# Kernel optimization log

Hardware: AMD Instinct MI355X
Metric: run time of the kernel (lower is better)

## Reference

```python
import jax, jax.numpy as jnp
import numpy as np

B, INP, OUP, FGROUP, H, W = 32, 256, 256, 8, 64, 64
CG = INP // FGROUP  # channels per group in GLGF fc1 layers


def conv3x3(x, w):
    # x: (N,1,H,W), w: (1,1,3,3); stride 1, padding 1 (SAME)
    return jax.lax.conv_general_dilated(
        x, w, window_strides=(1, 1), padding='SAME',
        dimension_numbers=('NCHW', 'OIHW', 'NCHW'))


def setup_inputs() -> dict:
    key = jax.random.key(0)
    ks = jax.random.split(key, 8)
    return {
        'x': jax.random.normal(ks[0], (B, INP, H, W), dtype=jnp.float32),
        # GLGF params (all 1x1 convs, bias=False), stored as dense matrices
        'w1l': jax.random.normal(ks[1], (FGROUP, CG, CG), dtype=jnp.float32) * 0.05,   # wn_fc1_l (groups=fgroup)
        'w1g1': jax.random.normal(ks[2], (FGROUP, CG), dtype=jnp.float32) * 0.05,      # wn_fc1_g1 (inp->fgroup, groups=fgroup)
        'w1g2': jax.random.normal(ks[3], (INP, FGROUP), dtype=jnp.float32) * 0.05,     # wn_fc1_g2 (fgroup->inp dense)
        'w2l': jax.random.normal(ks[4], (INP, OUP), dtype=jnp.float32) * 0.05,         # wn_fc2_l (groups=inp): input ch i -> oup outputs
        'w2g': jax.random.normal(ks[5], (INP,), dtype=jnp.float32) * 0.05,             # wn_fc2_g (inp->1 dense)
        'conv1_w': jax.random.normal(ks[6], (1, 1, 3, 3), dtype=jnp.float32) * 0.1,
        'conv2_w': jax.random.normal(ks[7], (1, 1, 3, 3), dtype=jnp.float32) * 0.1,
    }


def reference(x, w1l, w1g1, w1g2, w2l, w2g, conv1_w, conv2_w):
    b, c, h, w_ = x.shape
    fgroup, cg, _ = w1l.shape
    oup = w2l.shape[1]

    # adaptive_avg_pool2d(x, (1,1)) -> (B, inp) descriptor
    g = x.mean(axis=(2, 3))                                   # (B, inp)
    gg = g.reshape(b, fgroup, cg)

    # GLGF: fc1_l (grouped) + fc1_g2(fc1_g1) (squeeze to fgroup then expand)
    local = jnp.einsum('bgi,goi->bgo', gg, w1l).reshape(b, c)  # (B, inp)
    glob = jnp.einsum('bgi,gi->bg', gg, w1g1) @ w1g2.T         # (B, inp)
    s = jax.nn.sigmoid(local + glob)                           # (B, inp)

    # fc2_l (groups=inp): torch channel order is (input_ch g, out j) -> g*oup + j
    # fc2_g adds a per-sample scalar to every channel
    xw = s[:, :, None] * w2l + (s @ w2g)[:, None, None]        # (B, inp, oup)
    # WA_1Conv reinterprets the flat (oup*inp) channels as (oup, inp)
    Wdyn = xw.reshape(b, oup, c)                               # (B, oup, inp)

    # grouped conv with groups=batch, ksize=1 == per-sample matmul
    y = jnp.einsum('bihw,boi->bohw', x, Wdyn)                  # (B, oup, H, W)

    # channel gating: mean over channels -> conv3x3 -> sigmoid -> conv3x3
    cmap = y.mean(axis=1, keepdims=True)                       # (B, 1, H, W)
    cmap = conv3x3(cmap, conv1_w)
    cmap = jax.nn.sigmoid(cmap)
    cmap = conv3x3(cmap, conv2_w)
    return y * cmap
```

## Files before the change

### kernel.cpp

```cpp
#include <hip/hip_runtime.h>
#include <hip/hip_bf16.h>

typedef float  f32x4  __attribute__((ext_vector_type(4)));
typedef short  bf16x8 __attribute__((ext_vector_type(8)));

__device__ __forceinline__ short f2bf(float f) {
    union { __hip_bfloat16 h; short s; } u;
    u.h = __float2bfloat16(f);
    return u.s;
}

__device__ __forceinline__ void gload_lds16(const void* g, void* l) {
    __builtin_amdgcn_global_load_lds(
        (const __attribute__((address_space(1))) unsigned int*)g,
        (__attribute__((address_space(3))) unsigned int*)l, 16, 0, 0);
}

__device__ __forceinline__ void nt_load8(const float* p, float* dst) {
    const f32x4* vp = reinterpret_cast<const f32x4*>(p);
    f32x4 a = __builtin_nontemporal_load(vp);
    f32x4 b = __builtin_nontemporal_load(vp + 1);
    *reinterpret_cast<f32x4*>(dst)     = a;
    *reinterpret_cast<f32x4*>(dst + 4) = b;
}

__global__ __launch_bounds__(256) void transpose_kernel(const float* __restrict__ x,
                                                        short* __restrict__ xt,
                                                        float* __restrict__ gpart,
                                                        float* __restrict__ xsump) {
    const int pchunk = blockIdx.x;
    const int cchunk = blockIdx.y;
    const int c0 = cchunk * 64;
    const int b  = blockIdx.z;
    const int tid = threadIdx.x;
    const int cpair = tid >> 3;
    const int poct  = tid & 7;
    const int p0 = pchunk * 64;

    __shared__ unsigned int tile[64 * 32];
    __shared__ float xred[4 * 64];

    const float* rowA = x + ((size_t)(b * 256 + c0 + 2 * cpair)) * 4096 + p0 + poct * 8;
    const float* rowB = rowA + 4096;
    float av[8], bv[8];
    nt_load8(rowA, av);
    nt_load8(rowB, bv);

    float sA = 0.f, sB = 0.f;
    #pragma unroll
    for (int e = 0; e < 8; ++e) { sA += av[e]; sB += bv[e]; }
    sA += __shfl_xor(sA, 1, 64); sA += __shfl_xor(sA, 2, 64); sA += __shfl_xor(sA, 4, 64);
    sB += __shfl_xor(sB, 1, 64); sB += __shfl_xor(sB, 2, 64); sB += __shfl_xor(sB, 4, 64);
    if (poct == 0) {
        gpart[((size_t)(b * 256 + c0 + 2 * cpair)) * 64 + pchunk] = sA;
        gpart[((size_t)(b * 256 + c0 + 2 * cpair + 1)) * 64 + pchunk] = sB;
    }

    float xs[8];
    #pragma unroll
    for (int e = 0; e < 8; ++e) {
        float v = av[e] + bv[e];
        v += __shfl_xor(v, 8, 64);
        v += __shfl_xor(v, 16, 64);
        v += __shfl_xor(v, 32, 64);
        xs[e] = v;
    }
    if ((tid & 56) == 0) {
        int wv = tid >> 6;
        #pragma unroll
        for (int e = 0; e < 8; ++e) xred[wv * 64 + poct * 8 + e] = xs[e];
    }

    const int s = cpair >> 2, w = cpair & 3;
    #pragma unroll
    for (int e = 0; e < 8; ++e) {
        int p = poct * 8 + e;
        unsigned int u = (unsigned int)(unsigned short)f2bf(av[e]) |
                         ((unsigned int)(unsigned short)f2bf(bv[e]) << 16);
        tile[p * 32 + ((s ^ poct) << 2) + w] = u;
    }
    __syncthreads();

    if (tid < 64) {
        float v = xred[tid] + xred[64 + tid] + xred[128 + tid] + xred[192 + tid];
        xsump[((size_t)(cchunk * 32 + b)) * 4096 + p0 + tid] = v;
    }

    const int so = tid & 7;
    #pragma unroll
    for (int h = 0; h < 2; ++h) {
        int p = (tid >> 3) + h * 32;
        int sp = so ^ ((p >> 3) & 7);
        uint4 v = *reinterpret_cast<const uint4*>(&tile[p * 32 + sp * 4]);
        *reinterpret_cast<uint4*>(xt + ((size_t)b * 4096 + p0 + p) * 256 + c0 + so * 8) = v;
    }
}

__global__ __launch_bounds__(256) void prep_kernel(
    const float* __restrict__ gpart, const float* __restrict__ w1l,
    const float* __restrict__ w1g1, const float* __restrict__ w1g2,
    const float* __restrict__ w2l, const float* __restrict__ w2g,
    float* __restrict__ s_out, float* __restrict__ t_out,
    float* __restrict__ vq_out, short* __restrict__ w2l_bf) {
    int b = blockIdx.x;
    int tid = threadIdx.x;
    if (b >= 32) {
        int seg = b - 32;
        const float* src = w2l + seg * 4096;
        short* dst = w2l_bf + seg * 4096;
        #pragma unroll
        for (int it = 0; it < 4; ++it) {
            float4 v = *reinterpret_cast<const float4*>(src + it * 1024 + tid * 4);
            short4 o;
            o.x = f2bf(v.x); o.y = f2bf(v.y); o.z = f2bf(v.z); o.w = f2bf(v.w);
            *reinterpret_cast<short4*>(dst + it * 1024 + tid * 4) = o;
        }
        return;
    }
    __shared__ float gs[256];
    __shared__ float zs[8];
    __shared__ float ss[256];
    __shared__ float red[4];
    {
        const float4* gp = reinterpret_cast<const float4*>(gpart + (size_t)(b * 256 + tid) * 64);
        float acc = 0.f;
        #pragma unroll
        for (int j = 0; j < 16; ++j) { float4 v = gp[j]; acc += v.x + v.y + v.z + v.w; }
        gs[tid] = acc * (1.0f / 4096.0f);
    }
    __syncthreads();
    if (tid < 8) {
        float z = 0.f;
        for (int i = 0; i < 32; ++i) z += gs[tid * 32 + i] * w1g1[tid * 32 + i];
        zs[tid] = z;
    }
    __syncthreads();
    int grp = tid >> 5, o = tid & 31;
    float local = 0.f;
    #pragma unroll 4
    for (int i = 0; i < 32; ++i) local += gs[grp * 32 + i] * w1l[grp * 1024 + o * 32 + i];
    float glob = 0.f;
    #pragma unroll
    for (int gg = 0; gg < 8; ++gg) glob += zs[gg] * w1g2[tid * 8 + gg];
    float sv = 1.0f / (1.0f + expf(-(local + glob)));
    ss[tid] = sv;
    s_out[b * 256 + tid] = sv;
    float tv = sv * w2g[tid];
    #pragma unroll
    for (int off = 32; off; off >>= 1) tv += __shfl_down(tv, off, 64);
    if ((tid & 63) == 0) red[tid >> 6] = tv;
    __syncthreads();
    float tb = red[0] + red[1] + red[2] + red[3];
    if (tid == 0) t_out[b] = tb;
    float v = 0.f;
    for (int o2 = 0; o2 < 256; ++o2) v += ss[o2] * w2l[o2 * 256 + tid];
    vq_out[b * 256 + tid] = v * (1.0f / 256.0f);
}

__global__ __launch_bounds__(256) void cmap0_kernel(const short* __restrict__ xt,
                                                    const float* __restrict__ vq,
                                                    const float* __restrict__ t,
                                                    const float* __restrict__ xsump,
                                                    float* __restrict__ cmap0,
                                                    float* __restrict__ txs) {
    const int b = blockIdx.y;
    const int p = blockIdx.x * 256 + threadIdx.x;
    __shared__ float vs[256];
    vs[threadIdx.x] = vq[b * 256 + threadIdx.x];
    __syncthreads();
    const uint4* row = reinterpret_cast<const uint4*>(xt + ((size_t)b * 4096 + p) * 256);
    float acc = 0.f;
    #pragma unroll 8
    for (int it = 0; it < 32; ++it) {
        uint4 u = row[it];
        const unsigned int* uw = reinterpret_cast<const unsigned int*>(&u);
        #pragma unroll
        for (int j = 0; j < 4; ++j) {
            unsigned int wrd = uw[j];
            union { unsigned int u; float f; } lo, hi;
            lo.u = wrd << 16;
            hi.u = wrd & 0xffff0000u;
            acc += lo.f * vs[it * 8 + 2 * j] + hi.f * vs[it * 8 + 2 * j + 1];
        }
    }
    float xs = 0.f;
    #pragma unroll
    for (int part = 0; part < 4; ++part)
        xs += xsump[((size_t)(part * 32 + b)) * 4096 + p];
    float tb = t[b];
    float tx = tb * xs;
    cmap0[b * 4096 + p] = acc + tx;
    txs[b * 4096 + p] = tx;
}

__global__ __launch_bounds__(256) void convs_kernel(const float* __restrict__ cmap0,
                                                    const float* __restrict__ w9a,
                                                    const float* __restrict__ w9b,
                                                    float* __restrict__ cmap) {
    const int strip = blockIdx.x;
    const int b = blockIdx.y;
    const int tid = threadIdx.x;
    const int r0 = strip * 8;
    const int rlo = (r0 == 0) ? 0 : r0 - 1;
    const int rhi = (r0 + 8 > 63) ? 63 : r0 + 8;
    const int cnt = rhi - rlo + 1;

    __shared__ float mid[10 * 64];
    float wa[9], wb[9];
    #pragma unroll
    for (int i = 0; i < 9; ++i) { wa[i] = w9a[i]; wb[i] = w9b[i]; }
    const float* ib = cmap0 + (size_t)b * 4096;

    for (int idx = tid; idx < cnt * 64; idx += 256) {
        int r = rlo + (idx >> 6), cc = idx & 63;
        float acc = 0.f;
        #pragma unroll
        for (int dy = -1; dy <= 1; ++dy)
            #pragma unroll
            for (int dx = -1; dx <= 1; ++dx) {
                int rr = r + dy, xx = cc + dx;
                if (rr >= 0 && rr < 64 && xx >= 0 && xx < 64)
                    acc += ib[rr * 64 + xx] * wa[(dy + 1) * 3 + (dx + 1)];
            }
        mid[idx] = 1.0f / (1.0f + expf(-acc));
    }
    __syncthreads();
    for (int idx = tid; idx < 512; idx += 256) {
        int r = r0 + (idx >> 6), cc = idx & 63;
        float acc = 0.f;
        #pragma unroll
        for (int dy = -1; dy <= 1; ++dy)
            #pragma unroll
            for (int dx = -1; dx <= 1; ++dx) {
                int rr = r + dy, xx = cc + dx;
                if (rr >= 0 && rr < 64 && xx >= 0 && xx < 64)
                    acc += mid[(rr - rlo) * 64 + xx] * wb[(dy + 1) * 3 + (dx + 1)];
            }
        cmap[(size_t)b * 4096 + r * 64 + cc] = acc;
    }
}

__global__ __launch_bounds__(512) void gemm_epi_kernel(
    const short* __restrict__ xt, const short* __restrict__ w2l_bf,
    const float* __restrict__ s, const float* __restrict__ txs,
    const float* __restrict__ cmap, float* __restrict__ out) {
    const int b  = blockIdx.z;
    const int p0 = blockIdx.x * 64;
    const int tid  = threadIdx.x;
    const int lane = tid & 63;
    const int w    = tid >> 6;
    const int wm = w >> 1, wn = w & 1;

    __shared__ short Alds[2][256 * 64];
    __shared__ short Xlds[2][64 * 64];

    const int sl   = (lane & 7) ^ (lane >> 3);
    const int lrow = lane >> 3;

    float txr[2], cmr[2], sv[4][4];
    #pragma unroll
    for (int n = 0; n < 2; ++n) {
        int p = p0 + wn * 32 + n * 16 + (lane & 15);
        txr[n] = txs[b * 4096 + p];
        cmr[n] = cmap[b * 4096 + p];
    }
    #pragma unroll
    for (int m = 0; m < 4; ++m)
        #pragma unroll
        for (int r = 0; r < 4; ++r)
            sv[m][r] = s[b * 256 + wm * 64 + m * 16 + (lane >> 4) * 4 + r];

    f32x4 acc[4][2] = {};

    auto STAGE = [&](int bi, int ks) {
        #pragma unroll
        for (int j = 0; j < 4; ++j) {
            int chunk = w * 4 + j;
            int row = chunk * 8 + lrow;
            gload_lds16(w2l_bf + (size_t)row * 256 + ks + sl * 8,
                        (char*)(&Alds[bi][0]) + chunk * 1024);
        }
        int prow = w * 8 + lrow;
        gload_lds16(xt + ((size_t)b * 4096 + p0 + prow) * 256 + ks + sl * 8,
                    (char*)(&Xlds[bi][0]) + w * 1024);
    };

    STAGE(0, 0);
    #pragma unroll
    for (int t = 0; t < 4; ++t) {
        const int bi = t & 1;
        if (t < 3) {
            STAGE(bi ^ 1, (t + 1) * 64);
            asm volatile("s_waitcnt vmcnt(5)" ::: "memory");
        } else {
            asm volatile("s_waitcnt vmcnt(0)" ::: "memory");
        }
        __builtin_amdgcn_s_barrier();
        asm volatile("" ::: "memory");
        #pragma unroll
        for (int kk = 0; kk < 2; ++kk) {
            bf16x8 af[4], bfr[2];
            const int ss = kk * 4 + (lane >> 4);
            #pragma unroll
            for (int m = 0; m < 4; ++m) {
                int o = wm * 64 + m * 16 + (lane & 15);
                af[m] = *reinterpret_cast<const bf16x8*>(
                    (char*)(&Alds[bi][0]) + o * 128 + ((ss ^ (lane & 7)) * 16));
            }
            #pragma unroll
            for (int n = 0; n < 2; ++n) {
                int p = wn * 32 + n * 16 + (lane & 15);
                bfr[n] = *reinterpret_cast<const bf16x8*>(
                    (char*)(&Xlds[bi][0]) + p * 128 + ((ss ^ (lane & 7)) * 16));
            }
            #pragma unroll
            for (int m = 0; m < 4; ++m)
                #pragma unroll
                for (int n = 0; n < 2; ++n)
                    acc[m][n] = __builtin_amdgcn_mfma_f32_16x16x32_bf16(af[m], bfr[n], acc[m][n], 0, 0, 0);
        }
        asm volatile("" ::: "memory");
        __builtin_amdgcn_s_barrier();
    }
    #pragma unroll
    for (int n = 0; n < 2; ++n) {
        int p = p0 + wn * 32 + n * 16 + (lane & 15);
        #pragma unroll
        for (int m = 0; m < 4; ++m) {
            #pragma unroll
            for (int r = 0; r < 4; ++r) {
                int o = wm * 64 + m * 16 + (lane >> 4) * 4 + r;
                float yv = (sv[m][r] * acc[m][n][r] + txr[n]) * cmr[n];
                __builtin_nontemporal_store(yv, &out[((size_t)b * 256 + o) * 4096 + p]);
            }
        }
    }
}

extern "C" void kernel_launch(void* const* d_in, const int* in_sizes, int n_in,
                              void* d_out, int out_size, void* d_ws, size_t ws_size,
                              hipStream_t stream) {
    const float* x       = (const float*)d_in[0];
    const float* w1l     = (const float*)d_in[1];
    const float* w1g1    = (const float*)d_in[2];
    const float* w1g2    = (const float*)d_in[3];
    const float* w2l     = (const float*)d_in[4];
    const float* w2g     = (const float*)d_in[5];
    const float* conv1_w = (const float*)d_in[6];
    const float* conv2_w = (const float*)d_in[7];
    float* out = (float*)d_out;

    float* wsf    = (float*)d_ws;
    float* s      = wsf;
    float* t      = wsf + 8192;
    float* vq     = wsf + 8256;
    float* cmap0  = wsf + 16448;
    float* txs    = wsf + 147520;
    float* cmap   = wsf + 278592;
    float* gpart  = wsf + 409664;
    float* xsump  = wsf + 933952;
    short* w2l_bf = (short*)(wsf + 1458240);
    short* xt     = (short*)(wsf + 1491008);

    transpose_kernel<<<dim3(64, 4, 32), 256, 0, stream>>>(x, xt, gpart, xsump);
    prep_kernel<<<48, 256, 0, stream>>>(gpart, w1l, w1g1, w1g2, w2l, w2g, s, t, vq, w2l_bf);
    cmap0_kernel<<<dim3(16, 32), 256, 0, stream>>>(xt, vq, t, xsump, cmap0, txs);
    convs_kernel<<<dim3(8, 32), 256, 0, stream>>>(cmap0, conv1_w, conv2_w, cmap);
    gemm_epi_kernel<<<dim3(64, 1, 32), 512, 0, stream>>>(xt, w2l_bf, s, txs, cmap, out);
}
```

Before: 119.0 us.

## Fuse prep into cmap0 kernel and fold 3x3 convs into GEMM epilogue

Merges the per-sample prep kernel into the cmap0 kernel. Each of the 16 blocks per sample now recomputes s, t and vq redundantly instead of reading them from a separate launch. The two 3x3 gating convolutions move into the GEMM epilogue: each block loads five rows of cmap0 and computes its own row of cmap in LDS. This cuts five launches to three and drops intermediate buffers, at the cost of redundant prep work (including a 256x256 matvec per block) and an extra LDS phase after the GEMM.

```diff
diff --git a/kernel.cpp b/kernel.cpp
--- a/kernel.cpp
+++ b/kernel.cpp
@@ -96,16 +96,17 @@
     }
 }
 
-__global__ __launch_bounds__(256) void prep_kernel(
-    const float* __restrict__ gpart, const float* __restrict__ w1l,
-    const float* __restrict__ w1g1, const float* __restrict__ w1g2,
-    const float* __restrict__ w2l, const float* __restrict__ w2g,
-    float* __restrict__ s_out, float* __restrict__ t_out,
-    float* __restrict__ vq_out, short* __restrict__ w2l_bf) {
-    int b = blockIdx.x;
-    int tid = threadIdx.x;
+__global__ __launch_bounds__(256) void prep_cmap0_kernel(
+    const short* __restrict__ xt, const float* __restrict__ gpart,
+    const float* __restrict__ w1l, const float* __restrict__ w1g1,
+    const float* __restrict__ w1g2, const float* __restrict__ w2l,
+    const float* __restrict__ w2g, const float* __restrict__ xsump,
+    float* __restrict__ s_out, short* __restrict__ w2l_bf,
+    float* __restrict__ cmap0, float* __restrict__ txs) {
+    const int b = blockIdx.y;
+    const int tid = threadIdx.x;
     if (b >= 32) {
-        int seg = b - 32;
+        int seg = blockIdx.x;
         const float* src = w2l + seg * 4096;
         short* dst = w2l_bf + seg * 4096;
         #pragma unroll
@@ -121,6 +122,7 @@
     __shared__ float zs[8];
     __shared__ float ss[256];
     __shared__ float red[4];
+    __shared__ float vs[256];
     {
         const float4* gp = reinterpret_cast<const float4*>(gpart + (size_t)(b * 256 + tid) * 64);
         float acc = 0.f;
@@ -135,39 +137,32 @@
         zs[tid] = z;
     }
     __syncthreads();
-    int grp = tid >> 5, o = tid & 31;
-    float local = 0.f;
-    #pragma unroll 4
-    for (int i = 0; i < 32; ++i) local += gs[grp * 32 + i] * w1l[grp * 1024 + o * 32 + i];
-    float glob = 0.f;
-    #pragma unroll
-    for (int gg = 0; gg < 8; ++gg) glob += zs[gg] * w1g2[tid * 8 + gg];
-    float sv = 1.0f / (1.0f + expf(-(local + glob)));
-    ss[tid] = sv;
-    s_out[b * 256 + tid] = sv;
-    float tv = sv * w2g[tid];
-    #pragma unroll
-    for (int off = 32; off; off >>= 1) tv += __shfl_down(tv, off, 64);
-    if ((tid & 63) == 0) red[tid >> 6] = tv;
-    __syncthreads();
-    float tb = red[0] + red[1] + red[2] + red[3];
-    if (tid == 0) t_out[b] = tb;
-    float v = 0.f;
-    for (int o2 = 0; o2 < 256; ++o2) v += ss[o2] * w2l[o2 * 256 + tid];
-    vq_out[b * 256 + tid] = v * (1.0f / 256.0f);
-}
-
-__global__ __launch_bounds__(256) void cmap0_kernel(const short* __restrict__ xt,
-                                                    const float* __restrict__ vq,
-                                                    const float* __restrict__ t,
-                                                    const float* __restrict__ xsump,
-                                                    float* __restrict__ cmap0,
-                                                    float* __restrict__ txs) {
-    const int b = blockIdx.y;
-    const int p = blockIdx.x * 256 + threadIdx.x;
-    __shared__ float vs[256];
-    vs[threadIdx.x] = vq[b * 256 + threadIdx.x];
-    __syncthreads();
+    {
+        int grp = tid >> 5, o = tid & 31;
+        float local = 0.f;
+        #pragma unroll 4
+        for (int i = 0; i < 32; ++i) local += gs[grp * 32 + i] * w1l[grp * 1024 + o * 32 + i];
+        float glob = 0.f;
+        #pragma unroll
+        for (int gg = 0; gg < 8; ++gg) glob += zs[gg] * w1g2[tid * 8 + gg];
+        float sv = 1.0f / (1.0f + expf(-(local + glob)));
+        ss[tid] = sv;
+        if (blockIdx.x == 0) s_out[b * 256 + tid] = sv;
+        float tv = sv * w2g[tid];
+        #pragma unroll
+        for (int off = 32; off; off >>= 1) tv += __shfl_down(tv, off, 64);
+        if ((tid & 63) == 0) red[tid >> 6] = tv;
+    }
+    __syncthreads();
+    const float tb = red[0] + red[1] + red[2] + red[3];
+    {
+        float v = 0.f;
+        for (int o2 = 0; o2 < 256; ++o2) v += ss[o2] * w2l[o2 * 256 + tid];
+        vs[tid] = v * (1.0f / 256.0f);
+    }
+    __syncthreads();
+
+    const int p = blockIdx.x * 256 + tid;
     const uint4* row = reinterpret_cast<const uint4*>(xt + ((size_t)b * 4096 + p) * 256);
     float acc = 0.f;
     #pragma unroll 8
@@ -183,69 +178,23 @@
             acc += lo.f * vs[it * 8 + 2 * j] + hi.f * vs[it * 8 + 2 * j + 1];
         }
     }
-    float xs = 0.f;
+    float xsv = 0.f;
     #pragma unroll
     for (int part = 0; part < 4; ++part)
-        xs += xsump[((size_t)(part * 32 + b)) * 4096 + p];
-    float tb = t[b];
-    float tx = tb * xs;
+        xsv += xsump[((size_t)(part * 32 + b)) * 4096 + p];
+    float tx = tb * xsv;
     cmap0[b * 4096 + p] = acc + tx;
     txs[b * 4096 + p] = tx;
-}
-
-__global__ __launch_bounds__(256) void convs_kernel(const float* __restrict__ cmap0,
-                                                    const float* __restrict__ w9a,
-                                                    const float* __restrict__ w9b,
-                                                    float* __restrict__ cmap) {
-    const int strip = blockIdx.x;
-    const int b = blockIdx.y;
-    const int tid = threadIdx.x;
-    const int r0 = strip * 8;
-    const int rlo = (r0 == 0) ? 0 : r0 - 1;
-    const int rhi = (r0 + 8 > 63) ? 63 : r0 + 8;
-    const int cnt = rhi - rlo + 1;
-
-    __shared__ float mid[10 * 64];
-    float wa[9], wb[9];
-    #pragma unroll
-    for (int i = 0; i < 9; ++i) { wa[i] = w9a[i]; wb[i] = w9b[i]; }
-    const float* ib = cmap0 + (size_t)b * 4096;
-
-    for (int idx = tid; idx < cnt * 64; idx += 256) {
-        int r = rlo + (idx >> 6), cc = idx & 63;
-        float acc = 0.f;
-        #pragma unroll
-        for (int dy = -1; dy <= 1; ++dy)
-            #pragma unroll
-            for (int dx = -1; dx <= 1; ++dx) {
-                int rr = r + dy, xx = cc + dx;
-                if (rr >= 0 && rr < 64 && xx >= 0 && xx < 64)
-                    acc += ib[rr * 64 + xx] * wa[(dy + 1) * 3 + (dx + 1)];
-            }
-        mid[idx] = 1.0f / (1.0f + expf(-acc));
-    }
-    __syncthreads();
-    for (int idx = tid; idx < 512; idx += 256) {
-        int r = r0 + (idx >> 6), cc = idx & 63;
-        float acc = 0.f;
-        #pragma unroll
-        for (int dy = -1; dy <= 1; ++dy)
-            #pragma unroll
-            for (int dx = -1; dx <= 1; ++dx) {
-                int rr = r + dy, xx = cc + dx;
-                if (rr >= 0 && rr < 64 && xx >= 0 && xx < 64)
-                    acc += mid[(rr - rlo) * 64 + xx] * wb[(dy + 1) * 3 + (dx + 1)];
-            }
-        cmap[(size_t)b * 4096 + r * 64 + cc] = acc;
-    }
 }
 
 __global__ __launch_bounds__(512) void gemm_epi_kernel(
     const short* __restrict__ xt, const short* __restrict__ w2l_bf,
     const float* __restrict__ s, const float* __restrict__ txs,
-    const float* __restrict__ cmap, float* __restrict__ out) {
+    const float* __restrict__ cmap0, const float* __restrict__ w9a,
+    const float* __restrict__ w9b, float* __restrict__ out) {
     const int b  = blockIdx.z;
-    const int p0 = blockIdx.x * 64;
+    const int r  = blockIdx.x;
+    const int p0 = r * 64;
     const int tid  = threadIdx.x;
     const int lane = tid & 63;
     const int w    = tid >> 6;
@@ -257,18 +206,26 @@
     const int sl   = (lane & 7) ^ (lane >> 3);
     const int lrow = lane >> 3;
 
-    float txr[2], cmr[2], sv[4][4];
+    float wa[9], wb[9];
+    #pragma unroll
+    for (int i = 0; i < 9; ++i) { wa[i] = w9a[i]; wb[i] = w9b[i]; }
+    float c0v = 0.f;
+    if (tid < 320) {
+        int i5 = tid >> 6, cc = tid & 63;
+        int rr = r - 2 + i5;
+        if (rr >= 0 && rr < 64) c0v = cmap0[(size_t)b * 4096 + rr * 64 + cc];
+    }
+    float txr[2], sv[4][4];
     #pragma unroll
     for (int n = 0; n < 2; ++n) {
         int p = p0 + wn * 32 + n * 16 + (lane & 15);
         txr[n] = txs[b * 4096 + p];
-        cmr[n] = cmap[b * 4096 + p];
     }
     #pragma unroll
     for (int m = 0; m < 4; ++m)
         #pragma unroll
-        for (int r = 0; r < 4; ++r)
-            sv[m][r] = s[b * 256 + wm * 64 + m * 16 + (lane >> 4) * 4 + r];
+        for (int q = 0; q < 4; ++q)
+            sv[m][q] = s[b * 256 + wm * 64 + m * 16 + (lane >> 4) * 4 + q];
 
     f32x4 acc[4][2] = {};
 
@@ -322,15 +279,56 @@
         asm volatile("" ::: "memory");
         __builtin_amdgcn_s_barrier();
     }
+
+    __syncthreads();
+    float* csc  = (float*)&Alds[0][0];
+    float* midl = csc + 320;
+    float* cmsl = midl + 192;
+    if (tid < 320) csc[tid] = c0v;
+    __syncthreads();
+    if (tid < 192) {
+        int i3 = tid >> 6, cc = tid & 63;
+        int rm = r - 1 + i3;
+        float a = 0.f;
+        if (rm >= 0 && rm < 64) {
+            #pragma unroll
+            for (int dy = 0; dy < 3; ++dy)
+                #pragma unroll
+                for (int dx = -1; dx <= 1; ++dx) {
+                    int c2 = cc + dx;
+                    if (c2 >= 0 && c2 < 64)
+                        a += csc[(i3 + dy) * 64 + c2] * wa[dy * 3 + dx + 1];
+                }
+            a = 1.0f / (1.0f + expf(-a));
+        }
+        midl[tid] = a;
+    }
+    __syncthreads();
+    if (tid < 64) {
+        float a = 0.f;
+        #pragma unroll
+        for (int i3 = 0; i3 < 3; ++i3)
+            #pragma unroll
+            for (int dx = -1; dx <= 1; ++dx) {
+                int c2 = tid + dx;
+                if (c2 >= 0 && c2 < 64)
+                    a += midl[i3 * 64 + c2] * wb[i3 * 3 + dx + 1];
+            }
+        cmsl[tid] = a;
+    }
+    __syncthreads();
+
     #pragma unroll
     for (int n = 0; n < 2; ++n) {
-        int p = p0 + wn * 32 + n * 16 + (lane & 15);
+        int pc = wn * 32 + n * 16 + (lane & 15);
+        int p = p0 + pc;
+        float cm = cmsl[pc];
         #pragma unroll
         for (int m = 0; m < 4; ++m) {
             #pragma unroll
-            for (int r = 0; r < 4; ++r) {
-                int o = wm * 64 + m * 16 + (lane >> 4) * 4 + r;
-                float yv = (sv[m][r] * acc[m][n][r] + txr[n]) * cmr[n];
+            for (int q = 0; q < 4; ++q) {
+                int o = wm * 64 + m * 16 + (lane >> 4) * 4 + q;
+                float yv = (sv[m][q] * acc[m][n][q] + txr[n]) * cm;
                 __builtin_nontemporal_store(yv, &out[((size_t)b * 256 + o) * 4096 + p]);
             }
         }
@@ -352,19 +350,16 @@
 
     float* wsf    = (float*)d_ws;
     float* s      = wsf;
-    float* t      = wsf + 8192;
-    float* vq     = wsf + 8256;
-    float* cmap0  = wsf + 16448;
-    float* txs    = wsf + 147520;
-    float* cmap   = wsf + 278592;
-    float* gpart  = wsf + 409664;
-    float* xsump  = wsf + 933952;
-    short* w2l_bf = (short*)(wsf + 1458240);
-    short* xt     = (short*)(wsf + 1491008);
+    float* cmap0  = wsf + 8192;
+    float* txs    = wsf + 139264;
+    float* gpart  = wsf + 270336;
+    float* xsump  = wsf + 794624;
+    short* w2l_bf = (short*)(wsf + 1318912);
+    short* xt     = (short*)(wsf + 1351680);
 
     transpose_kernel<<<dim3(64, 4, 32), 256, 0, stream>>>(x, xt, gpart, xsump);
-    prep_kernel<<<48, 256, 0, stream>>>(gpart, w1l, w1g1, w1g2, w2l, w2g, s, t, vq, w2l_bf);
-    cmap0_kernel<<<dim3(16, 32), 256, 0, stream>>>(xt, vq, t, xsump, cmap0, txs);
-    convs_kernel<<<dim3(8, 32), 256, 0, stream>>>(cmap0, conv1_w, conv2_w, cmap);
-    gemm_epi_kernel<<<dim3(64, 1, 32), 512, 0, stream>>>(xt, w2l_bf, s, txs, cmap, out);
-}
+    prep_cmap0_kernel<<<dim3(16, 33), 256, 0, stream>>>(
+        xt, gpart, w1l, w1g1, w1g2, w2l, w2g, xsump, s, w2l_bf, cmap0, txs);
+    gemm_epi_kernel<<<dim3(64, 1, 32), 512, 0, stream>>>(
+        xt, w2l_bf, s, txs, cmap0, conv1_w, conv2_w, out);
+}
```

New measurement: 118.7 us, median of 2. About the same (-0.2%).
